# Performance work log

Measured on AMD Instinct MI355X. Metric: run time of the kernel, lower is better.

Reference implementation:

```python
import jax, jax.numpy as jnp
import numpy as np

B, T, D = 2, 2048, 768
H, DH = 12, 64  # heads, head_dim; H*DH == D


def setup_inputs() -> dict:
    key = jax.random.key(0)
    ks = jax.random.split(key, 9)
    s = 0.02  # small init scale like GPT-2
    return {
        "x": jax.random.normal(ks[0], (B, T, D), dtype=jnp.float32),
        "Wq": jax.random.normal(ks[1], (D, H * DH), dtype=jnp.float32) * s,
        "bq": jax.random.normal(ks[2], (H * DH,), dtype=jnp.float32) * s,
        "Wk": jax.random.normal(ks[3], (D, H * DH), dtype=jnp.float32) * s,
        "bk": jax.random.normal(ks[4], (H * DH,), dtype=jnp.float32) * s,
        "Wv": jax.random.normal(ks[5], (D, H * DH), dtype=jnp.float32) * s,
        "bv": jax.random.normal(ks[6], (H * DH,), dtype=jnp.float32) * s,
        "Wo": jax.random.normal(ks[7], (H * DH, H * DH), dtype=jnp.float32) * s,
        "bo": jax.random.normal(ks[8], (H * DH,), dtype=jnp.float32) * s,
    }


def reference(x, Wq, bq, Wk, bk, Wv, bv, Wo, bo):
    b, t, _ = x.shape
    # projections -> [b, t, H, DH] -> [b, H, t, DH]
    q = (x @ Wq + bq).reshape(b, t, H, DH).transpose(0, 2, 1, 3)
    k = (x @ Wk + bk).reshape(b, t, H, DH).transpose(0, 2, 1, 3)
    v = (x @ Wv + bv).reshape(b, t, H, DH).transpose(0, 2, 1, 3)
    # full O(T^2) score matrix, matching the naive torch module
    scores = jnp.einsum("bhqd,bhkd->bhqk", q, k)
    causal = jnp.tril(jnp.ones((t, t), dtype=bool))  # True = keep
    scores = jnp.where(causal, scores, -jnp.inf)
    weights = jax.nn.softmax(scores / jnp.sqrt(jnp.float32(DH)), axis=-1)
    # dropout with p=0.0 is identity
    ctx = jnp.einsum("bhqk,bhkd->bhqd", weights, v)
    ctx = ctx.transpose(0, 2, 1, 3).reshape(b, t, H * DH)
    return ctx @ Wo + bo
```

## Files before the change

### kernel.cpp

```cpp
#include <hip/hip_runtime.h>
#include <hip/hip_bf16.h>
#include <math.h>

typedef unsigned short u16;
typedef unsigned int u32;
typedef __attribute__((ext_vector_type(8))) short short8v;
typedef __attribute__((ext_vector_type(4))) float f32x4;
typedef __attribute__((ext_vector_type(16))) float f32x16;

#define BB 2
#define TT 2048
#define DD 768
#define HH 12
#define DHH 64
#define MM 4096
#define NSLOT 36
#define QSC 0.18033688f

#define SWZ(r, kb) (((r) * 128) + ((kb) ^ (((r) & 7) << 4)))

typedef __attribute__((address_space(1))) void gas_void;
typedef __attribute__((address_space(3))) void las_void;
#define GLL(g, l) __builtin_amdgcn_global_load_lds((gas_void*)(g), (las_void*)(l), 16, 0, 0)

__device__ const unsigned char SLOT_QT[36] = {
    7,7,7,7,7,7,7, 6,6,6,6,6,6, 5,5,5,5,5, 4,4,4,4, 3,3,3, 2,2, 1,
    7,6,5,4,3,2,1,0};
__device__ const unsigned char SLOT_C[36] = {
    0,1,2,3,4,5,6, 0,1,2,3,4,5, 0,1,2,3,4, 0,1,2,3, 0,1,2, 0,1, 0,
    7,6,5,4,3,2,1,0};
__device__ const unsigned char BASEF[8] = {0, 27, 25, 22, 18, 13, 7, 0};

__device__ __forceinline__ u16 f2bf(float f) {
    union { float f; unsigned u; } v; v.f = f;
    unsigned r = v.u + 0x7fff + ((v.u >> 16) & 1);
    return (u16)(r >> 16);
}
__device__ __forceinline__ u32 pkpair(float a, float b) {
    union { __hip_bfloat162 h; u32 u; } v;
    v.h = __float22bfloat162_rn(make_float2(a, b));
    return v.u;
}
__device__ __forceinline__ float fexp2(float x) {
#if __has_builtin(__builtin_amdgcn_exp2f)
    return __builtin_amdgcn_exp2f(x);
#else
    return exp2f(x);
#endif
}
__device__ __forceinline__ float bfhi(u32 p) {
    union { u32 u; float f; } v; v.u = p & 0xffff0000u; return v.f;
}
__device__ __forceinline__ float bflo(u32 p) {
    union { u32 u; float f; } v; v.u = p << 16; return v.f;
}

__global__ __launch_bounds__(256) void prep(
    const float* __restrict__ x, u16* __restrict__ xb,
    const float* __restrict__ W0, const float* __restrict__ W1,
    const float* __restrict__ W2, const float* __restrict__ W3,
    u16* __restrict__ T0, u16* __restrict__ T1,
    u16* __restrict__ T2, u16* __restrict__ T3)
{
    __shared__ float tile[64][65];
    const int bid = blockIdx.x;
    const int t = threadIdx.x;

    if (bid < 3072) {
        const int i = bid * 256 + t;
        const float4 v = ((const float4*)x)[i];
        union { u16 s[4]; uint2 u; } o;
        o.s[0] = f2bf(v.x); o.s[1] = f2bf(v.y); o.s[2] = f2bf(v.z); o.s[3] = f2bf(v.w);
        ((uint2*)xb)[i] = o.u;
        return;
    }

    const int idx = bid - 3072;
    const int z = idx / 144;
    const int r2 = idx - z * 144;
    const int k0 = (r2 / 12) * 64, n0 = (r2 % 12) * 64;
    const float* __restrict__ W = (z == 0) ? W0 : (z == 1) ? W1 : (z == 2) ? W2 : W3;
    u16* __restrict__ T = (z == 0) ? T0 : (z == 1) ? T1 : (z == 2) ? T2 : T3;

    const int rr = t >> 4, c4 = (t & 15) * 4;
    #pragma unroll
    for (int j = 0; j < 4; ++j) {
        const int r = rr + j * 16;
        const float4 v = *(const float4*)&W[(size_t)(k0 + r) * DD + n0 + c4];
        tile[r][c4 + 0] = v.x; tile[r][c4 + 1] = v.y;
        tile[r][c4 + 2] = v.z; tile[r][c4 + 3] = v.w;
    }
    __syncthreads();
    #pragma unroll
    for (int j = 0; j < 4; ++j) {
        const int r = rr + j * 16;
        union { u16 s[4]; uint2 u; } o;
        #pragma unroll
        for (int jj = 0; jj < 4; ++jj) o.s[jj] = f2bf(tile[c4 + jj][r]);
        *(uint2*)&T[(size_t)(n0 + r) * DD + k0 + c4] = o.u;
    }
}

__global__ __launch_bounds__(256) void gemm_bt(
    const u16* __restrict__ A,
    const u16* __restrict__ Bt0, const u16* __restrict__ Bt1, const u16* __restrict__ Bt2,
    const float* __restrict__ b0, const float* __restrict__ b1, const float* __restrict__ b2,
    u16* __restrict__ oQ, u16* __restrict__ oK, u16* __restrict__ oVt,
    float* __restrict__ oF, int mode_base)
{
    const int mode = mode_base + blockIdx.z;
    const u16* __restrict__ Bt = (mode == 1) ? Bt1 : (mode == 2) ? Bt2 : Bt0;
    const float* __restrict__ bias = (mode == 1) ? b1 : (mode == 2) ? b2 : b0;

    __shared__ __attribute__((aligned(16))) unsigned char AsB[2][16384];
    __shared__ __attribute__((aligned(16))) unsigned char BsB[2][16384];

    const int tid = threadIdx.x, lane = tid & 63, w = tid >> 6;
    const int wr = w >> 1, wc = w & 1;
    const int lr = lane >> 4, lc = lane & 15;
    const int m0 = blockIdx.x * 128, n0 = blockIdx.y * 128;
    const int srcoff = 16 * ((lane & 7) ^ (lane >> 3));

#define GSTAGE(k0_, bufi) do {                                                 \
        _Pragma("unroll")                                                      \
        for (int i_ = 0; i_ < 4; ++i_) {                                       \
            const int r_ = w * 32 + i_ * 8 + (lane >> 3);                      \
            GLL((const char*)A  + ((size_t)(m0 + r_) * DD + (k0_)) * 2 + srcoff,\
                (char*)AsB[bufi] + w * 4096 + i_ * 1024);                      \
            GLL((const char*)Bt + ((size_t)(n0 + r_) * DD + (k0_)) * 2 + srcoff,\
                (char*)BsB[bufi] + w * 4096 + i_ * 1024);                      \
        }                                                                      \
    } while (0)

    f32x4 acc[4][4];
    #pragma unroll
    for (int m = 0; m < 4; ++m)
        #pragma unroll
        for (int n = 0; n < 4; ++n) acc[m][n] = (f32x4){0.f, 0.f, 0.f, 0.f};

    GSTAGE(0, 0);
    __syncthreads();

    int cur = 0;
    #pragma unroll 1
    for (int k0 = 0; k0 < DD; k0 += 64) {
        if (k0 + 64 < DD) GSTAGE(k0 + 64, cur ^ 1);

        #pragma unroll
        for (int s = 0; s < 2; ++s) {
            short8v af[4], bf[4];
            #pragma unroll
            for (int m = 0; m < 4; ++m)
                af[m] = *(const short8v*)((const char*)AsB[cur] +
                         SWZ(wr * 64 + m * 16 + lc, s * 64 + lr * 16));
            #pragma unroll
            for (int n = 0; n < 4; ++n)
                bf[n] = *(const short8v*)((const char*)BsB[cur] +
                         SWZ(wc * 64 + n * 16 + lc, s * 64 + lr * 16));
            #pragma unroll
            for (int m = 0; m < 4; ++m)
                #pragma unroll
                for (int n = 0; n < 4; ++n)
                    acc[m][n] = __builtin_amdgcn_mfma_f32_16x16x32_bf16(
                        af[m], bf[n], acc[m][n], 0, 0, 0);
        }

        __syncthreads();
        cur ^= 1;
    }
#undef GSTAGE

    #pragma unroll
    for (int n = 0; n < 4; ++n) {
        const int ng = n0 + wc * 64 + n * 16 + lc;
        const float bv = bias[ng];
        #pragma unroll
        for (int m = 0; m < 4; ++m) {
            const int mg0 = m0 + wr * 64 + m * 16 + lr * 4;
            if (mode == 3) {
                #pragma unroll
                for (int r = 0; r < 4; ++r)
                    oF[(size_t)(mg0 + r) * DD + ng] = acc[m][n][r] + bv;
            } else if (mode == 2) {
                const int bb = mg0 >> 11, tp = mg0 & 2047;
                const int h = ng >> 6, d = ng & 63;
                const size_t idx = (size_t)(bb * HH + h) * (TT * DHH)
                                 + (tp >> 6) * 4096 + ((tp >> 3) & 7) * 512
                                 + d * 8 + (tp & 7);
                union { u16 s[4]; uint2 u; } o;
                #pragma unroll
                for (int r = 0; r < 4; ++r) o.s[r] = f2bf(acc[m][n][r] + bv);
                *(uint2*)&oVt[idx] = o.u;
            } else if (mode == 1) {
                const int h = ng >> 6, d = ng & 63;
                #pragma unroll
                for (int r = 0; r < 4; ++r) {
                    const int mg = mg0 + r;
                    const int bb = mg >> 11, tp = mg & 2047;
                    oK[(size_t)(bb * HH + h) * (TT * DHH)
                       + (tp >> 6) * 4096 + (d >> 3) * 512 + (tp & 63) * 8 + (d & 7)] =
                        f2bf(acc[m][n][r] + bv);
                }
            } else {
                const int h = ng >> 6, d = ng & 63;
                #pragma unroll
                for (int r = 0; r < 4; ++r) {
                    const int mg = mg0 + r;
                    const int bb = mg >> 11, tp = mg & 2047;
                    oQ[((size_t)(bb * HH + h) * TT + tp) * DHH + d] =
                        f2bf((acc[m][n][r] + bv) * QSC);
                }
            }
        }
    }
}

__global__ __launch_bounds__(512) void attn_fwd(
    const u16* __restrict__ qb, const u16* __restrict__ kbf,
    const u16* __restrict__ vtb, u16* __restrict__ partO,
    float* __restrict__ partL)
{
    __shared__ __attribute__((aligned(16))) unsigned char smem[65536];

    const int bid = blockIdx.x;
    const int sp = bid / 24;
    const int bh = bid - sp * 24;
    const int qt = SLOT_QT[sp], c = SLOT_C[sp];
    const int kts = c * 4;

    const int tid = threadIdx.x, lane = tid & 63, w = tid >> 6;
    const int l31 = lane & 31, hi = lane >> 5;

    {
        const char* kbase = (const char*)kbf + (size_t)bh * (TT * DHH * 2)
                          + (size_t)kts * 8192;
        const char* vbase = (const char*)vtb + (size_t)bh * (TT * DHH * 2)
                          + (size_t)kts * 8192;
        const int off = w * 1024;
        #pragma unroll
        for (int t = 0; t < 4; ++t) {
            GLL(kbase + t * 8192 + off + lane * 16,
                (char*)smem + t * 8192 + off);
            GLL(vbase + t * 8192 + off + lane * 16,
                (char*)smem + 32768 + t * 8192 + off);
        }
    }

    short8v aq[4];
    {
        const u16* qrow = qb + ((size_t)bh * TT + qt * 256 + w * 32 + l31) * DHH;
        #pragma unroll
        for (int s4 = 0; s4 < 4; ++s4)
            aq[s4] = *(const short8v*)(qrow + s4 * 16 + hi * 8);
    }

    f32x16 accO[2];
    #pragma unroll
    for (int i = 0; i < 16; ++i) { accO[0][i] = 0.f; accO[1][i] = 0.f; }
    float lreg = 0.f;

    __syncthreads();

    const int qmin = qt * 256 + w * 32;
    #pragma unroll
    for (int t = 0; t < 4; ++t) {
        const int kt = kts + t;
        if (kt * 64 <= qmin + 31) {
            const unsigned char* Kb = smem + t * 8192;
            const unsigned char* Vb = smem + 32768 + t * 8192;

            f32x16 st[2];
            #pragma unroll
            for (int i = 0; i < 16; ++i) { st[0][i] = 0.f; st[1][i] = 0.f; }
            __builtin_amdgcn_s_setprio(1);
            #pragma unroll
            for (int s4 = 0; s4 < 4; ++s4) {
                #pragma unroll
                for (int kf = 0; kf < 2; ++kf) {
                    const short8v ak = *(const short8v*)(Kb +
                        (s4 * 2 + hi) * 1024 + (kf * 32 + l31) * 16);
                    st[kf] = __builtin_amdgcn_mfma_f32_32x32x16_bf16(ak, aq[s4], st[kf], 0, 0, 0);
                }
            }
            __builtin_amdgcn_s_setprio(0);

            if (kt * 64 + 63 > qmin) {
                const int rowrel = qmin + l31 - kt * 64;
                #pragma unroll
                for (int kf = 0; kf < 2; ++kf)
                    #pragma unroll
                    for (int reg = 0; reg < 16; ++reg) {
                        const int kloc = kf * 32 + (reg & 3) + 8 * (reg >> 2) + 4 * hi;
                        if (kloc > rowrel) st[kf][reg] = -3.0e38f;
                    }
            }

            float rs4[4] = {0.f, 0.f, 0.f, 0.f};
            #pragma unroll
            for (int kf = 0; kf < 2; ++kf)
                #pragma unroll
                for (int reg = 0; reg < 16; ++reg) {
                    const float p = fexp2(st[kf][reg]);
                    st[kf][reg] = p;
                    rs4[reg & 3] += p;
                }
            float rs = (rs4[0] + rs4[1]) + (rs4[2] + rs4[3]);
            {
                u32 a, b;
                union { float f; u32 u; } cv; cv.f = rs;
                a = cv.u; b = cv.u;
                asm volatile("v_permlane32_swap_b32 %0, %1" : "+v"(a), "+v"(b));
                union { u32 u; float f; } pa, pb; pa.u = a; pb.u = b;
                const float partner = hi ? pa.f : pb.f;
                rs += partner;
            }
            lreg += rs;

            __builtin_amdgcn_s_setprio(1);
            #pragma unroll
            for (int ka = 0; ka < 4; ++ka) {
                const int kf = ka >> 1;
                const int rb0 = 4 * ((ka & 1) * 2);
                const int rb1 = 4 * ((ka & 1) * 2 + 1);
                u32 P0 = pkpair(st[kf][rb0 + 0], st[kf][rb0 + 1]);
                u32 P1 = pkpair(st[kf][rb0 + 2], st[kf][rb0 + 3]);
                u32 Q0 = pkpair(st[kf][rb1 + 0], st[kf][rb1 + 1]);
                u32 Q1 = pkpair(st[kf][rb1 + 2], st[kf][rb1 + 3]);
                asm volatile("v_permlane32_swap_b32 %0, %1" : "+v"(P0), "+v"(Q0));
                asm volatile("v_permlane32_swap_b32 %0, %1" : "+v"(P1), "+v"(Q1));
                union { u32 wd[4]; short8v v; } u;
                u.wd[0] = P0; u.wd[1] = P1; u.wd[2] = Q0; u.wd[3] = Q1;
                #pragma unroll
                for (int dc = 0; dc < 2; ++dc) {
                    const short8v bv = *(const short8v*)(Vb +
                        (ka * 2 + hi) * 1024 + (dc * 32 + l31) * 16);
                    accO[dc] = __builtin_amdgcn_mfma_f32_32x32x16_bf16(u.v, bv, accO[dc], 0, 0, 0);
                }
            }
            __builtin_amdgcn_s_setprio(0);
        }
    }

    const int gslot = bh * NSLOT + sp;
    if (hi == 0)
        partL[(size_t)gslot * 256 + w * 32 + l31] = lreg;
    u16* po = partO + (size_t)gslot * 16384;
    #pragma unroll
    for (int reg = 0; reg < 16; ++reg) {
        const int qrow = (reg & 3) + 8 * (reg >> 2) + 4 * hi;
        #pragma unroll
        for (int dc = 0; dc < 2; ++dc)
            po[(w * 32 + qrow) * 64 + dc * 32 + l31] = f2bf(accO[dc][reg]);
    }
}

__global__ __launch_bounds__(256) void attn_combine(
    const u16* __restrict__ partO, const float* __restrict__ partL,
    u16* __restrict__ ctx)
{
    const int bid = blockIdx.x;
    const int q64 = bid / 24, bh = bid - q64 * 24;
    const int b = bh / HH, h = bh - b * HH;
    const int qt = q64 >> 2;
    const int sub = q64 & 3;
    const int tid = threadIdx.x, q = tid >> 2, dg = tid & 3;
    const int prow = sub * 64 + q;

    float lsum = 0.f;
    float acc[16];
    #pragma unroll
    for (int j = 0; j < 16; ++j) acc[j] = 0.f;

#define ACCUM(gs) do {                                                         \
        lsum += partL[(size_t)(gs) * 256 + prow];                              \
        const u16* po_ = partO + (size_t)(gs) * 16384 + prow * 64 + dg * 16;   \
        _Pragma("unroll")                                                      \
        for (int v_ = 0; v_ < 2; ++v_) {                                       \
            const uint4 pk = *(const uint4*)(po_ + v_ * 8);                    \
            acc[v_*8+0] += bflo(pk.x); acc[v_*8+1] += bfhi(pk.x);              \
            acc[v_*8+2] += bflo(pk.y); acc[v_*8+3] += bfhi(pk.y);              \
            acc[v_*8+4] += bflo(pk.z); acc[v_*8+5] += bfhi(pk.z);              \
            acc[v_*8+6] += bflo(pk.w); acc[v_*8+7] += bfhi(pk.w);              \
        }                                                                      \
    } while (0)

    const int basef = bh * NSLOT + BASEF[qt];
    #pragma unroll 1
    for (int cc = 0; cc < qt; ++cc) ACCUM(basef + cc);
    ACCUM(bh * NSLOT + (35 - qt));
#undef ACCUM

    const float inv = 1.f / lsum;
    u16* dst = ctx + (size_t)(b * TT + qt * 256 + prow) * DD + h * 64 + dg * 16;
    #pragma unroll
    for (int v = 0; v < 2; ++v) {
        uint4 o;
        o.x = pkpair(acc[v*8+0] * inv, acc[v*8+1] * inv);
        o.y = pkpair(acc[v*8+2] * inv, acc[v*8+3] * inv);
        o.z = pkpair(acc[v*8+4] * inv, acc[v*8+5] * inv);
        o.w = pkpair(acc[v*8+6] * inv, acc[v*8+7] * inv);
        *(uint4*)(dst + v * 8) = o;
    }
}

extern "C" void kernel_launch(void* const* d_in, const int* in_sizes, int n_in,
                              void* d_out, int out_size, void* d_ws, size_t ws_size,
                              hipStream_t stream) {
    (void)in_sizes; (void)n_in; (void)out_size; (void)ws_size;
    const float* x  = (const float*)d_in[0];
    const float* Wq = (const float*)d_in[1];
    const float* bq = (const float*)d_in[2];
    const float* Wk = (const float*)d_in[3];
    const float* bk = (const float*)d_in[4];
    const float* Wv = (const float*)d_in[5];
    const float* bv = (const float*)d_in[6];
    const float* Wo = (const float*)d_in[7];
    const float* bo = (const float*)d_in[8];
    float* out = (float*)d_out;

    u16* xb    = (u16*)d_ws;
    u16* WtQ   = xb + (size_t)MM * DD;
    u16* WtK   = WtQ + (size_t)DD * DD;
    u16* WtV   = WtK + (size_t)DD * DD;
    u16* WtO   = WtV + (size_t)DD * DD;
    u16* qbuf  = WtO + (size_t)DD * DD;
    u16* kbuf  = qbuf + (size_t)MM * DD;
    u16* vtbuf = kbuf + (size_t)MM * DD;
    u16* ctxb  = vtbuf + (size_t)MM * DD;
    u16* pO    = ctxb + (size_t)MM * DD;
    float* pL  = (float*)(pO + (size_t)24 * NSLOT * 16384);

    prep<<<dim3(3648), 256, 0, stream>>>(x, xb, Wq, Wk, Wv, Wo, WtQ, WtK, WtV, WtO);
    gemm_bt<<<dim3(32, 6, 3), 256, 0, stream>>>(xb, WtQ, WtK, WtV, bq, bk, bv,
                                                qbuf, kbuf, vtbuf, nullptr, 0);
    attn_fwd<<<dim3(24 * NSLOT), 512, 0, stream>>>(qbuf, kbuf, vtbuf, pO, pL);
    attn_combine<<<dim3(768), 256, 0, stream>>>(pO, pL, ctxb);
    gemm_bt<<<dim3(32, 6, 1), 256, 0, stream>>>(ctxb, WtO, nullptr, nullptr, bo, nullptr, nullptr,
                                                nullptr, nullptr, nullptr, out, 3);
}
```

Baseline: 90.58 us.

## Swizzle QKV GEMM block order and use 64-row tiles for output projection

The QKV projection GEMM now runs on a 1D grid. Block indices are remapped with a stride-8 swizzle so that co-resident blocks share the same A rows across Q, K and V, which should improve L2 and XCD locality. The output projection moves to a dedicated kernel with 64x128 tiles, giving 384 blocks instead of 192 to fill the GPU's CUs better. The cost is smaller tiles with lower arithmetic intensity, and more A/B reloads per output.

```diff
diff --git a/kernel.cpp b/kernel.cpp
--- a/kernel.cpp
+++ b/kernel.cpp
@@ -105,10 +105,16 @@
     const u16* __restrict__ A,
     const u16* __restrict__ Bt0, const u16* __restrict__ Bt1, const u16* __restrict__ Bt2,
     const float* __restrict__ b0, const float* __restrict__ b1, const float* __restrict__ b2,
-    u16* __restrict__ oQ, u16* __restrict__ oK, u16* __restrict__ oVt,
-    float* __restrict__ oF, int mode_base)
+    u16* __restrict__ oQ, u16* __restrict__ oK, u16* __restrict__ oVt)
 {
-    const int mode = mode_base + blockIdx.z;
+    const int lin = blockIdx.x;
+    const int cpx = gridDim.x >> 3;
+    const int swz = (lin & 7) * cpx + (lin >> 3);
+    const int mt  = swz / 18;
+    const int r18 = swz - mt * 18;
+    const int mode = r18 / 6;
+    const int m0 = mt * 128, n0 = (r18 - mode * 6) * 128;
+
     const u16* __restrict__ Bt = (mode == 1) ? Bt1 : (mode == 2) ? Bt2 : Bt0;
     const float* __restrict__ bias = (mode == 1) ? b1 : (mode == 2) ? b2 : b0;
 
@@ -118,7 +124,6 @@
     const int tid = threadIdx.x, lane = tid & 63, w = tid >> 6;
     const int wr = w >> 1, wc = w & 1;
     const int lr = lane >> 4, lc = lane & 15;
-    const int m0 = blockIdx.x * 128, n0 = blockIdx.y * 128;
     const int srcoff = 16 * ((lane & 7) ^ (lane >> 3));
 
 #define GSTAGE(k0_, bufi) do {                                                 \
@@ -177,11 +182,7 @@
         #pragma unroll
         for (int m = 0; m < 4; ++m) {
             const int mg0 = m0 + wr * 64 + m * 16 + lr * 4;
-            if (mode == 3) {
-                #pragma unroll
-                for (int r = 0; r < 4; ++r)
-                    oF[(size_t)(mg0 + r) * DD + ng] = acc[m][n][r] + bv;
-            } else if (mode == 2) {
+            if (mode == 2) {
                 const int bb = mg0 >> 11, tp = mg0 & 2047;
                 const int h = ng >> 6, d = ng & 63;
                 const size_t idx = (size_t)(bb * HH + h) * (TT * DHH)
@@ -211,6 +212,91 @@
                         f2bf((acc[m][n][r] + bv) * QSC);
                 }
             }
+        }
+    }
+}
+
+__global__ __launch_bounds__(256) void gemm_out64(
+    const u16* __restrict__ A, const u16* __restrict__ Bt,
+    const float* __restrict__ bias, float* __restrict__ oF)
+{
+    const int lin = blockIdx.x;
+    const int cpx = gridDim.x >> 3;
+    const int swz = (lin & 7) * cpx + (lin >> 3);
+    const int m0 = (swz / 6) * 64;
+    const int n0 = (swz % 6) * 128;
+
+    __shared__ __attribute__((aligned(16))) unsigned char AsB[2][8192];
+    __shared__ __attribute__((aligned(16))) unsigned char BsB[2][16384];
+
+    const int tid = threadIdx.x, lane = tid & 63, w = tid >> 6;
+    const int wr = w >> 1, wc = w & 1;
+    const int lr = lane >> 4, lc = lane & 15;
+    const int srcoff = 16 * ((lane & 7) ^ (lane >> 3));
+
+#define GSTAGE(k0_, bufi) do {                                                 \
+        _Pragma("unroll")                                                      \
+        for (int i_ = 0; i_ < 2; ++i_) {                                       \
+            const int ra_ = w * 16 + i_ * 8 + (lane >> 3);                     \
+            GLL((const char*)A  + ((size_t)(m0 + ra_) * DD + (k0_)) * 2 + srcoff,\
+                (char*)AsB[bufi] + w * 2048 + i_ * 1024);                      \
+        }                                                                      \
+        _Pragma("unroll")                                                      \
+        for (int i_ = 0; i_ < 4; ++i_) {                                       \
+            const int rb_ = w * 32 + i_ * 8 + (lane >> 3);                     \
+            GLL((const char*)Bt + ((size_t)(n0 + rb_) * DD + (k0_)) * 2 + srcoff,\
+                (char*)BsB[bufi] + w * 4096 + i_ * 1024);                      \
+        }                                                                      \
+    } while (0)
+
+    f32x4 acc[2][4];
+    #pragma unroll
+    for (int m = 0; m < 2; ++m)
+        #pragma unroll
+        for (int n = 0; n < 4; ++n) acc[m][n] = (f32x4){0.f, 0.f, 0.f, 0.f};
+
+    GSTAGE(0, 0);
+    __syncthreads();
+
+    int cur = 0;
+    #pragma unroll 1
+    for (int k0 = 0; k0 < DD; k0 += 64) {
+        if (k0 + 64 < DD) GSTAGE(k0 + 64, cur ^ 1);
+
+        #pragma unroll
+        for (int s = 0; s < 2; ++s) {
+            short8v af[2], bf[4];
+            #pragma unroll
+            for (int m = 0; m < 2; ++m)
+                af[m] = *(const short8v*)((const char*)AsB[cur] +
+                         SWZ(wr * 32 + m * 16 + lc, s * 64 + lr * 16));
+            #pragma unroll
+            for (int n = 0; n < 4; ++n)
+                bf[n] = *(const short8v*)((const char*)BsB[cur] +
+                         SWZ(wc * 64 + n * 16 + lc, s * 64 + lr * 16));
+            #pragma unroll
+            for (int m = 0; m < 2; ++m)
+                #pragma unroll
+                for (int n = 0; n < 4; ++n)
+                    acc[m][n] = __builtin_amdgcn_mfma_f32_16x16x32_bf16(
+                        af[m], bf[n], acc[m][n], 0, 0, 0);
+        }
+
+        __syncthreads();
+        cur ^= 1;
+    }
+#undef GSTAGE
+
+    #pragma unroll
+    for (int n = 0; n < 4; ++n) {
+        const int ng = n0 + wc * 64 + n * 16 + lc;
+        const float bv = bias[ng];
+        #pragma unroll
+        for (int m = 0; m < 2; ++m) {
+            const int mg0 = m0 + wr * 32 + m * 16 + lr * 4;
+            #pragma unroll
+            for (int r = 0; r < 4; ++r)
+                oF[(size_t)(mg0 + r) * DD + ng] = acc[m][n][r] + bv;
         }
     }
 }
@@ -431,10 +517,9 @@
     float* pL  = (float*)(pO + (size_t)24 * NSLOT * 16384);
 
     prep<<<dim3(3648), 256, 0, stream>>>(x, xb, Wq, Wk, Wv, Wo, WtQ, WtK, WtV, WtO);
-    gemm_bt<<<dim3(32, 6, 3), 256, 0, stream>>>(xb, WtQ, WtK, WtV, bq, bk, bv,
-                                                qbuf, kbuf, vtbuf, nullptr, 0);
+    gemm_bt<<<dim3(576), 256, 0, stream>>>(xb, WtQ, WtK, WtV, bq, bk, bv,
+                                           qbuf, kbuf, vtbuf);
     attn_fwd<<<dim3(24 * NSLOT), 512, 0, stream>>>(qbuf, kbuf, vtbuf, pO, pL);
     attn_combine<<<dim3(768), 256, 0, stream>>>(pO, pL, ctxb);
-    gemm_bt<<<dim3(32, 6, 1), 256, 0, stream>>>(ctxb, WtO, nullptr, nullptr, bo, nullptr, nullptr,
-                                                nullptr, nullptr, nullptr, out, 3);
-}
+    gemm_out64<<<dim3(384), 256, 0, stream>>>(ctxb, WtO, bo, out);
+}
```

Result: faster. 86.98 us (median of 3 runs) (-4.0%).
